# Performance work log

Hardware: AMD Instinct MI355X
Metric: run time of the kernel (lower is better)

The kernel has to match this reference:

```python
import jax, jax.numpy as jnp
import numpy as np


def setup_inputs() -> dict:
    key = jax.random.key(0)
    ks = jax.random.split(key, 5)
    Bsz, T, d = 8, 2048, 1024
    x = jax.random.normal(ks[0], (Bsz, T, d), dtype=jnp.float32)
    W_in = jax.random.normal(ks[1], (d, d), dtype=jnp.float32) * (1.0 / np.sqrt(d))
    b_in = jnp.zeros((d,), dtype=jnp.float32)
    log_A = -jnp.ones((d,), dtype=jnp.float32)  # keras Constant(-1.0) init
    B_vec = jax.random.normal(ks[2], (d,), dtype=jnp.float32) * 0.05  # keras random_normal stddev
    C = jax.random.normal(ks[3], (d, d), dtype=jnp.float32) * 0.05
    D = jnp.zeros((d,), dtype=jnp.float32)
    return {"x": x, "W_in": W_in, "b_in": b_in, "log_A": log_A, "B_vec": B_vec, "C": C, "D": D}


def reference(x, W_in, b_in, log_A, B_vec, C, D):
    # u = in_proj(x)
    u = jnp.einsum('btd,de->bte', x, W_in) + b_in            # [B,T,d]
    A = -jnp.exp(log_A)                                       # [d]
    # linear recurrence h_t = h_{t-1} * A + u_t * B, h_0 = 0
    # expressed as an associative scan over pairs (a_t, b_t):
    #   (a1,b1) o (a2,b2) = (a1*a2, b1*a2 + b2)
    b = u * B_vec                                             # [B,T,d]
    a = jnp.broadcast_to(A, b.shape)                          # [B,T,d]

    def combine(e1, e2):
        a1, b1 = e1
        a2, b2 = e2
        return (a1 * a2, b1 * a2 + b2)

    _, h_seq = jax.lax.associative_scan(combine, (a, b), axis=1)  # h_t, [B,T,d]
    y = jnp.einsum('bts,sd->btd', h_seq, C)
    return y + x * D
```

## Files before the change

### kernel.cpp

```cpp
#include <hip/hip_runtime.h>
#include <hip/hip_bf16.h>

typedef unsigned short ushort_t;
typedef __bf16 bf16x8 __attribute__((ext_vector_type(8)));
typedef float f32x4 __attribute__((ext_vector_type(4)));

#define BM 128
#define BN 128
#define BK 64

__device__ __forceinline__ float bf2f(ushort_t u) {
    union { unsigned int i; float f; } x; x.i = ((unsigned int)u) << 16; return x.f;
}
__device__ __forceinline__ ushort_t f2bf(float f) {
    __hip_bfloat16 h = __float2bfloat16(f);
    return *(ushort_t*)&h;
}
__device__ __forceinline__ void async16(const void* g, void* l) {
    __builtin_amdgcn_global_load_lds((const __attribute__((address_space(1))) void*)g,
                                     (__attribute__((address_space(3))) void*)l, 16, 0, 0);
}

__global__ void prep_fused(const float* __restrict__ x, const float* __restrict__ W_in,
                           const float* __restrict__ C, const float* __restrict__ Bv,
                           __hip_bfloat16* __restrict__ xb, __hip_bfloat16* __restrict__ Wpt,
                           __hip_bfloat16* __restrict__ Ct) {
    int bid = blockIdx.x;
    if (bid < 16384) {
        size_t idx = ((size_t)bid * 256 + threadIdx.x) * 4;
        float4 v = *(const float4*)(x + idx);
        ushort4 ov;
        ov.x = f2bf(v.x); ov.y = f2bf(v.y); ov.z = f2bf(v.z); ov.w = f2bf(v.w);
        *(ushort4*)((ushort_t*)xb + idx) = ov;
        return;
    }
    __shared__ float tile[32][33];
    const float* in;
    __hip_bfloat16* out;
    bool do_scale;
    int lid;
    if (bid < 17408) { lid = bid - 16384; in = W_in; out = Wpt; do_scale = true; }
    else             { lid = bid - 17408; in = C;    out = Ct;  do_scale = false; }
    int bx = (lid & 31) * 32;
    int by = (lid >> 5) * 32;
    int tx = threadIdx.x & 31, ty = threadIdx.x >> 5;
    #pragma unroll
    for (int i = 0; i < 32; i += 8)
        tile[ty + i][tx] = in[(size_t)(by + ty + i) * 1024 + bx + tx];
    __syncthreads();
    if (threadIdx.x < 128) {
        int n_local = threadIdx.x & 31;
        int quad    = threadIdx.x >> 5;
        int n = bx + n_local;
        float s = do_scale ? Bv[n] : 1.0f;
        int lr     = n & 15;
        int n_tile = n >> 4;
        int k_tile = by >> 5;
        ushort_t buf[8];
        #pragma unroll
        for (int j = 0; j < 8; ++j)
            buf[j] = f2bf(tile[quad * 8 + j][n_local] * s);
        size_t off = (((size_t)n_tile * 32 + k_tile) * 64 + quad * 16 + lr) * 8;
        ushort_t* dst = (ushort_t*)out + off;
        *(ushort4*)dst       = *(ushort4*)&buf[0];
        *(ushort4*)(dst + 4) = *(ushort4*)&buf[4];
    }
}

__global__ __launch_bounds__(256) void gemm1_scan(
    const __hip_bfloat16* __restrict__ Ab, const __hip_bfloat16* __restrict__ Bpk,
    const float* __restrict__ b_in, const float* __restrict__ Bv,
    const float* __restrict__ logA,
    __hip_bfloat16* __restrict__ hout, int M, int N, int K) {
    const int tid  = threadIdx.x;
    const int wave = tid >> 6;
    const int lane = tid & 63;
    const int quad = lane >> 4;
    const int lr   = lane & 15;
    const int wm   = wave >> 1;
    const int wn   = wave & 1;

    const int lin   = blockIdx.y * gridDim.x + blockIdx.x;
    const int xcd   = lin & 7;
    const int local = lin >> 3;
    const int m_blk = xcd * 16 + (local >> 3);
    const int n_blk = local & 7;
    const int m0 = m_blk * BM;
    const int n0 = n_blk * BN;

    __shared__ __align__(16) ushort_t sBuf[160 * 136];

    const ushort_t* A  = (const ushort_t*)Ab;
    const ushort_t* Bp = (const ushort_t*)Bpk;
    const int ktiles = K >> 5;
    const int ntile0 = n0 >> 4;

    f32x4 acc[5][4];
    #pragma unroll
    for (int i = 0; i < 5; ++i)
        #pragma unroll
        for (int j = 0; j < 4; ++j)
            #pragma unroll
            for (int r = 0; r < 4; ++r) acc[i][j][r] = 0.0f;

    const int row8 = lane >> 3;
    const int schunk = (lane & 7) ^ row8;
    const int ldcol = schunk * 8;
    for (int k0 = 0; k0 < K; k0 += BK) {
        __syncthreads();
        #pragma unroll
        for (int j = 0; j < 5; ++j) {
            int c = j * 4 + wave;
            int row = c * 8 + row8;
            int grow = m0 - 32 + row;
            if (grow < 0) grow = 0;
            const ushort_t* gA = A + (size_t)grow * K + k0 + ldcol;
            async16(gA, &sBuf[c * 512]);
        }
        __syncthreads();
        #pragma unroll
        for (int kk = 0; kk < BK; kk += 32) {
            const int kt = (k0 + kk) >> 5;
            bf16x8 bfr[4];
            #pragma unroll
            for (int j = 0; j < 4; ++j)
                bfr[j] = *(const bf16x8*)&Bp[((((size_t)(ntile0 + wn * 4 + j)) * ktiles + kt) * 64 + lane) * 8];
            const int ck = (kk >> 3) + quad;
            const int pc = (ck ^ (lr & 7)) * 8;
            bf16x8 af[5];
            #pragma unroll
            for (int i = 0; i < 5; ++i)
                af[i] = *(const bf16x8*)&sBuf[(wm * 80 + i * 16 + lr) * BK + pc];
            #pragma unroll
            for (int i = 0; i < 5; ++i)
                #pragma unroll
                for (int j = 0; j < 4; ++j)
                    acc[i][j] = __builtin_amdgcn_mfma_f32_16x16x32_bf16(af[i], bfr[j], acc[i][j], 0, 0, 0);
        }
    }

    __syncthreads();
    #pragma unroll
    for (int i = 0; i < 5; ++i)
        #pragma unroll
        for (int j = 0; j < 4; ++j) {
            int colL = wn * 64 + j * 16 + lr;
            float bs = b_in[n0 + colL] * Bv[n0 + colL];
            #pragma unroll
            for (int r = 0; r < 4; ++r) {
                int slot = wm * 80 + i * 16 + quad * 4 + r;
                sBuf[slot * 136 + colL] = f2bf(acc[i][j][r] + bs);
            }
        }
    __syncthreads();
    if (tid < 128) {
        float a = -__expf(logA[n0 + tid]);
        float h = 0.f;
        int s = ((m0 & 2047) == 0) ? 32 : 0;
        for (; s < 32; ++s)
            h = fmaf(a, h, bf2f(sBuf[s * 136 + tid]));
        #pragma unroll 4
        for (int t = 32; t < 160; ++t) {
            h = fmaf(a, h, bf2f(sBuf[t * 136 + tid]));
            sBuf[t * 136 + tid] = f2bf(h);
        }
    }
    __syncthreads();
    #pragma unroll
    for (int i = 0; i < 4; ++i) {
        int r32 = tid >> 3;
        int cch = (tid & 7) * 16;
        int slot = 32 + i * 32 + r32;
        bf16x8 v0 = *(const bf16x8*)&sBuf[slot * 136 + cch];
        bf16x8 v1 = *(const bf16x8*)&sBuf[slot * 136 + cch + 8];
        ushort_t* dst = (ushort_t*)hout + (size_t)(m0 + i * 32 + r32) * N + n0 + cch;
        *(bf16x8*)dst       = v0;
        *(bf16x8*)(dst + 8) = v1;
    }
}

__global__ __launch_bounds__(256) void gemm2(
    const __hip_bfloat16* __restrict__ Ab, const __hip_bfloat16* __restrict__ Bpk,
    const __hip_bfloat16* __restrict__ xres_bf, const float* __restrict__ Dvec,
    float* __restrict__ out_f, int M, int N, int K) {
    const int tid  = threadIdx.x;
    const int wave = tid >> 6;
    const int lane = tid & 63;
    const int quad = lane >> 4;
    const int lr   = lane & 15;
    const int wm   = wave >> 1;
    const int wn   = wave & 1;

    const int lin   = blockIdx.y * gridDim.x + blockIdx.x;
    const int xcd   = lin & 7;
    const int local = lin >> 3;
    const int m_blk = xcd * 16 + (local >> 3);
    const int n_blk = local & 7;
    const int m0 = m_blk * BM;
    const int n0 = n_blk * BN;

    __shared__ __align__(16) ushort_t sA[BM * BK];

    const ushort_t* A  = (const ushort_t*)Ab;
    const ushort_t* Bp = (const ushort_t*)Bpk;
    const int ktiles = K >> 5;
    const int ntile0 = n0 >> 4;

    f32x4 acc[4][4];
    #pragma unroll
    for (int i = 0; i < 4; ++i)
        #pragma unroll
        for (int j = 0; j < 4; ++j)
            #pragma unroll
            for (int r = 0; r < 4; ++r) acc[i][j][r] = 0.0f;

    const int row8 = lane >> 3;
    const int schunk = (lane & 7) ^ row8;
    const int ldcol = schunk * 8;
    for (int k0 = 0; k0 < K; k0 += BK) {
        __syncthreads();
        #pragma unroll
        for (int j = 0; j < 4; ++j) {
            int c = j * 4 + wave;
            int row = c * 8 + row8;
            const ushort_t* gA = A + (size_t)(m0 + row) * K + k0 + ldcol;
            async16(gA, &sA[c * 512]);
        }
        __syncthreads();
        #pragma unroll
        for (int kk = 0; kk < BK; kk += 32) {
            const int kt = (k0 + kk) >> 5;
            bf16x8 bfr[4];
            #pragma unroll
            for (int j = 0; j < 4; ++j)
                bfr[j] = *(const bf16x8*)&Bp[((((size_t)(ntile0 + wn * 4 + j)) * ktiles + kt) * 64 + lane) * 8];
            const int ck = (kk >> 3) + quad;
            const int pc = (ck ^ (lr & 7)) * 8;
            bf16x8 af[4];
            #pragma unroll
            for (int i = 0; i < 4; ++i)
                af[i] = *(const bf16x8*)&sA[(wm * 64 + i * 16 + lr) * BK + pc];
            #pragma unroll
            for (int i = 0; i < 4; ++i)
                #pragma unroll
                for (int j = 0; j < 4; ++j)
                    acc[i][j] = __builtin_amdgcn_mfma_f32_16x16x32_bf16(af[i], bfr[j], acc[i][j], 0, 0, 0);
        }
    }

    #pragma unroll
    for (int i = 0; i < 4; ++i) {
        int row = m0 + wm * 64 + i * 16 + quad * 4;
        #pragma unroll
        for (int j = 0; j < 4; ++j) {
            int col = n0 + wn * 64 + j * 16 + lr;
            float dv = Dvec[col];
            #pragma unroll
            for (int r = 0; r < 4; ++r) {
                float xv = bf2f(((const ushort_t*)xres_bf)[(size_t)(row + r) * N + col]);
                out_f[(size_t)(row + r) * N + col] = acc[i][j][r] + xv * dv;
            }
        }
    }
}

extern "C" void kernel_launch(void* const* d_in, const int* in_sizes, int n_in,
                              void* d_out, int out_size, void* d_ws, size_t ws_size,
                              hipStream_t stream) {
    const float* x    = (const float*)d_in[0];
    const float* W_in = (const float*)d_in[1];
    const float* b_in = (const float*)d_in[2];
    const float* logA = (const float*)d_in[3];
    const float* Bv   = (const float*)d_in[4];
    const float* C    = (const float*)d_in[5];
    const float* Dv   = (const float*)d_in[6];
    float* out = (float*)d_out;

    const int Bsz = 8, T = 2048, d = 1024;
    const int M = Bsz * T;

    char* w = (char*)d_ws;
    __hip_bfloat16* xb   = (__hip_bfloat16*)w;
    __hip_bfloat16* Wpt  = xb + (size_t)M * d;
    __hip_bfloat16* Ct   = Wpt + (size_t)d * d;
    __hip_bfloat16* hbuf = Ct + (size_t)d * d;

    prep_fused<<<16384 + 2048, 256, 0, stream>>>(x, W_in, C, Bv, xb, Wpt, Ct);

    gemm1_scan<<<dim3(d / BN, M / BM), 256, 0, stream>>>(
        xb, Wpt, b_in, Bv, logA, hbuf, M, d, d);
    gemm2<<<dim3(d / BN, M / BM), 256, 0, stream>>>(
        hbuf, Ct, xb, Dv, out, M, d, d);
}
```

Before: 241.3 us.

## Pre-pack activations into MFMA fragment layout and drop LDS staging in GEMMs

The prep kernel now writes x as bf16 in a pre-tiled MFMA fragment layout, and gemm1_scan likewise writes h in that layout. Both GEMMs can then load A and B fragments straight from global memory with contiguous 16-byte per-lane loads, with no LDS staging and no __syncthreads in the K loop. gemm2 reads the fp32 x residual directly instead of the bf16 copy. This removes LDS traffic and barriers, but makes A-tile reuse across waves rely on the L2 cache, and the residual read becomes twice as large.

```diff
diff --git a/kernel.cpp b/kernel.cpp
--- a/kernel.cpp
+++ b/kernel.cpp
@@ -5,10 +5,6 @@
 typedef __bf16 bf16x8 __attribute__((ext_vector_type(8)));
 typedef float f32x4 __attribute__((ext_vector_type(4)));
 
-#define BM 128
-#define BN 128
-#define BK 64
-
 __device__ __forceinline__ float bf2f(ushort_t u) {
     union { unsigned int i; float f; } x; x.i = ((unsigned int)u) << 16; return x.f;
 }
@@ -16,22 +12,35 @@
     __hip_bfloat16 h = __float2bfloat16(f);
     return *(ushort_t*)&h;
 }
-__device__ __forceinline__ void async16(const void* g, void* l) {
-    __builtin_amdgcn_global_load_lds((const __attribute__((address_space(1))) void*)g,
-                                     (__attribute__((address_space(3))) void*)l, 16, 0, 0);
-}
+
 
 __global__ void prep_fused(const float* __restrict__ x, const float* __restrict__ W_in,
                            const float* __restrict__ C, const float* __restrict__ Bv,
-                           __hip_bfloat16* __restrict__ xb, __hip_bfloat16* __restrict__ Wpt,
+                           __hip_bfloat16* __restrict__ xpk, __hip_bfloat16* __restrict__ Wpt,
                            __hip_bfloat16* __restrict__ Ct) {
     int bid = blockIdx.x;
-    if (bid < 16384) {
-        size_t idx = ((size_t)bid * 256 + threadIdx.x) * 4;
-        float4 v = *(const float4*)(x + idx);
-        ushort4 ov;
-        ov.x = f2bf(v.x); ov.y = f2bf(v.y); ov.z = f2bf(v.z); ov.w = f2bf(v.w);
-        *(ushort4*)((ushort_t*)xb + idx) = ov;
+    if (bid < 1024) {
+        __shared__ ushort_t sm[16 * 1032];
+        int tid = threadIdx.x;
+        #pragma unroll
+        for (int r = 0; r < 16; ++r) {
+            float4 v = *(const float4*)(x + ((size_t)(bid * 16 + r)) * 1024 + tid * 4);
+            ushort4 ov;
+            ov.x = f2bf(v.x); ov.y = f2bf(v.y); ov.z = f2bf(v.z); ov.w = f2bf(v.w);
+            *(ushort4*)&sm[r * 1032 + tid * 4] = ov;
+        }
+        __syncthreads();
+        int lane = tid & 63;
+        int quad = lane >> 4;
+        int lr   = lane & 15;
+        #pragma unroll
+        for (int p = 0; p < 8; ++p) {
+            int kt = p * 4 + (tid >> 6);
+            const ushort_t* src = &sm[lr * 1032 + kt * 32 + quad * 8];
+            ushort_t* dst = (ushort_t*)xpk + (((size_t)bid * 32 + kt) * 64 + lane) * 8;
+            *(ushort4*)dst       = *(const ushort4*)src;
+            *(ushort4*)(dst + 4) = *(const ushort4*)(src + 4);
+        }
         return;
     }
     __shared__ float tile[32][33];
@@ -39,8 +48,8 @@
     __hip_bfloat16* out;
     bool do_scale;
     int lid;
-    if (bid < 17408) { lid = bid - 16384; in = W_in; out = Wpt; do_scale = true; }
-    else             { lid = bid - 17408; in = C;    out = Ct;  do_scale = false; }
+    if (bid < 2048) { lid = bid - 1024; in = W_in; out = Wpt; do_scale = true; }
+    else            { lid = bid - 2048; in = C;    out = Ct;  do_scale = false; }
     int bx = (lid & 31) * 32;
     int by = (lid >> 5) * 32;
     int tx = threadIdx.x & 31, ty = threadIdx.x >> 5;
@@ -68,10 +77,10 @@
 }
 
 __global__ __launch_bounds__(256) void gemm1_scan(
-    const __hip_bfloat16* __restrict__ Ab, const __hip_bfloat16* __restrict__ Bpk,
+    const __hip_bfloat16* __restrict__ Apk, const __hip_bfloat16* __restrict__ Bpk,
     const float* __restrict__ b_in, const float* __restrict__ Bv,
     const float* __restrict__ logA,
-    __hip_bfloat16* __restrict__ hout, int M, int N, int K) {
+    __hip_bfloat16* __restrict__ hpk, int N) {
     const int tid  = threadIdx.x;
     const int wave = tid >> 6;
     const int lane = tid & 63;
@@ -85,15 +94,27 @@
     const int local = lin >> 3;
     const int m_blk = xcd * 16 + (local >> 3);
     const int n_blk = local & 7;
-    const int m0 = m_blk * BM;
-    const int n0 = n_blk * BN;
+    const int m0 = m_blk * 128;
+    const int n0 = n_blk * 128;
 
     __shared__ __align__(16) ushort_t sBuf[160 * 136];
 
-    const ushort_t* A  = (const ushort_t*)Ab;
+    const ushort_t* Ap = (const ushort_t*)Apk;
     const ushort_t* Bp = (const ushort_t*)Bpk;
-    const int ktiles = K >> 5;
-    const int ntile0 = n0 >> 4;
+
+    const ushort_t* pA[5];
+    const ushort_t* pB[4];
+    #pragma unroll
+    for (int i = 0; i < 5; ++i) {
+        int mt = (m0 >> 4) - 2 + wm * 5 + i;
+        if (mt < 0) mt = 0;
+        pA[i] = Ap + (size_t)mt * 32 * 512 + lane * 8;
+    }
+    #pragma unroll
+    for (int j = 0; j < 4; ++j) {
+        int nt = (n0 >> 4) + wn * 4 + j;
+        pB[j] = Bp + (size_t)nt * 32 * 512 + lane * 8;
+    }
 
     f32x4 acc[5][4];
     #pragma unroll
@@ -103,40 +124,18 @@
             #pragma unroll
             for (int r = 0; r < 4; ++r) acc[i][j][r] = 0.0f;
 
-    const int row8 = lane >> 3;
-    const int schunk = (lane & 7) ^ row8;
-    const int ldcol = schunk * 8;
-    for (int k0 = 0; k0 < K; k0 += BK) {
-        __syncthreads();
-        #pragma unroll
-        for (int j = 0; j < 5; ++j) {
-            int c = j * 4 + wave;
-            int row = c * 8 + row8;
-            int grow = m0 - 32 + row;
-            if (grow < 0) grow = 0;
-            const ushort_t* gA = A + (size_t)grow * K + k0 + ldcol;
-            async16(gA, &sBuf[c * 512]);
-        }
-        __syncthreads();
-        #pragma unroll
-        for (int kk = 0; kk < BK; kk += 32) {
-            const int kt = (k0 + kk) >> 5;
-            bf16x8 bfr[4];
+    #pragma unroll 2
+    for (int kt = 0; kt < 32; ++kt) {
+        bf16x8 af[5], bfr[4];
+        #pragma unroll
+        for (int i = 0; i < 5; ++i) af[i]  = *(const bf16x8*)(pA[i] + (size_t)kt * 512);
+        #pragma unroll
+        for (int j = 0; j < 4; ++j) bfr[j] = *(const bf16x8*)(pB[j] + (size_t)kt * 512);
+        #pragma unroll
+        for (int i = 0; i < 5; ++i)
             #pragma unroll
             for (int j = 0; j < 4; ++j)
-                bfr[j] = *(const bf16x8*)&Bp[((((size_t)(ntile0 + wn * 4 + j)) * ktiles + kt) * 64 + lane) * 8];
-            const int ck = (kk >> 3) + quad;
-            const int pc = (ck ^ (lr & 7)) * 8;
-            bf16x8 af[5];
-            #pragma unroll
-            for (int i = 0; i < 5; ++i)
-                af[i] = *(const bf16x8*)&sBuf[(wm * 80 + i * 16 + lr) * BK + pc];
-            #pragma unroll
-            for (int i = 0; i < 5; ++i)
-                #pragma unroll
-                for (int j = 0; j < 4; ++j)
-                    acc[i][j] = __builtin_amdgcn_mfma_f32_16x16x32_bf16(af[i], bfr[j], acc[i][j], 0, 0, 0);
-        }
+                acc[i][j] = __builtin_amdgcn_mfma_f32_16x16x32_bf16(af[i], bfr[j], acc[i][j], 0, 0, 0);
     }
 
     __syncthreads();
@@ -167,22 +166,23 @@
     }
     __syncthreads();
     #pragma unroll
-    for (int i = 0; i < 4; ++i) {
-        int r32 = tid >> 3;
-        int cch = (tid & 7) * 16;
-        int slot = 32 + i * 32 + r32;
-        bf16x8 v0 = *(const bf16x8*)&sBuf[slot * 136 + cch];
-        bf16x8 v1 = *(const bf16x8*)&sBuf[slot * 136 + cch + 8];
-        ushort_t* dst = (ushort_t*)hout + (size_t)(m0 + i * 32 + r32) * N + n0 + cch;
-        *(bf16x8*)dst       = v0;
-        *(bf16x8*)(dst + 8) = v1;
+    for (int p = 0; p < 8; ++p) {
+        int sb   = p * 4 + wave;
+        int mt_l = sb >> 2;
+        int kt_l = sb & 3;
+        const ushort_t* src = &sBuf[(32 + mt_l * 16 + lr) * 136 + kt_l * 32 + quad * 8];
+        size_t mt  = (size_t)((m0 >> 4) + mt_l);
+        size_t kt2 = (size_t)((n0 >> 5) + kt_l);
+        ushort_t* dst = (ushort_t*)hpk + ((mt * 32 + kt2) * 64 + lane) * 8;
+        *(ushort4*)dst       = *(const ushort4*)src;
+        *(ushort4*)(dst + 4) = *(const ushort4*)(src + 4);
     }
 }
 
 __global__ __launch_bounds__(256) void gemm2(
-    const __hip_bfloat16* __restrict__ Ab, const __hip_bfloat16* __restrict__ Bpk,
-    const __hip_bfloat16* __restrict__ xres_bf, const float* __restrict__ Dvec,
-    float* __restrict__ out_f, int M, int N, int K) {
+    const __hip_bfloat16* __restrict__ Apk, const __hip_bfloat16* __restrict__ Bpk,
+    const float* __restrict__ xres_f, const float* __restrict__ Dvec,
+    float* __restrict__ out_f, int N) {
     const int tid  = threadIdx.x;
     const int wave = tid >> 6;
     const int lane = tid & 63;
@@ -196,15 +196,20 @@
     const int local = lin >> 3;
     const int m_blk = xcd * 16 + (local >> 3);
     const int n_blk = local & 7;
-    const int m0 = m_blk * BM;
-    const int n0 = n_blk * BN;
-
-    __shared__ __align__(16) ushort_t sA[BM * BK];
-
-    const ushort_t* A  = (const ushort_t*)Ab;
+    const int m0 = m_blk * 128;
+    const int n0 = n_blk * 128;
+
+    const ushort_t* Ap = (const ushort_t*)Apk;
     const ushort_t* Bp = (const ushort_t*)Bpk;
-    const int ktiles = K >> 5;
-    const int ntile0 = n0 >> 4;
+
+    const ushort_t* pA[4];
+    const ushort_t* pB[4];
+    #pragma unroll
+    for (int i = 0; i < 4; ++i)
+        pA[i] = Ap + (size_t)((m0 >> 4) + wm * 4 + i) * 32 * 512 + lane * 8;
+    #pragma unroll
+    for (int j = 0; j < 4; ++j)
+        pB[j] = Bp + (size_t)((n0 >> 4) + wn * 4 + j) * 32 * 512 + lane * 8;
 
     f32x4 acc[4][4];
     #pragma unroll
@@ -214,38 +219,18 @@
             #pragma unroll
             for (int r = 0; r < 4; ++r) acc[i][j][r] = 0.0f;
 
-    const int row8 = lane >> 3;
-    const int schunk = (lane & 7) ^ row8;
-    const int ldcol = schunk * 8;
-    for (int k0 = 0; k0 < K; k0 += BK) {
-        __syncthreads();
-        #pragma unroll
-        for (int j = 0; j < 4; ++j) {
-            int c = j * 4 + wave;
-            int row = c * 8 + row8;
-            const ushort_t* gA = A + (size_t)(m0 + row) * K + k0 + ldcol;
-            async16(gA, &sA[c * 512]);
-        }
-        __syncthreads();
-        #pragma unroll
-        for (int kk = 0; kk < BK; kk += 32) {
-            const int kt = (k0 + kk) >> 5;
-            bf16x8 bfr[4];
+    #pragma unroll 2
+    for (int kt = 0; kt < 32; ++kt) {
+        bf16x8 af[4], bfr[4];
+        #pragma unroll
+        for (int i = 0; i < 4; ++i) af[i]  = *(const bf16x8*)(pA[i] + (size_t)kt * 512);
+        #pragma unroll
+        for (int j = 0; j < 4; ++j) bfr[j] = *(const bf16x8*)(pB[j] + (size_t)kt * 512);
+        #pragma unroll
+        for (int i = 0; i < 4; ++i)
             #pragma unroll
             for (int j = 0; j < 4; ++j)
-                bfr[j] = *(const bf16x8*)&Bp[((((size_t)(ntile0 + wn * 4 + j)) * ktiles + kt) * 64 + lane) * 8];
-            const int ck = (kk >> 3) + quad;
-            const int pc = (ck ^ (lr & 7)) * 8;
-            bf16x8 af[4];
-            #pragma unroll
-            for (int i = 0; i < 4; ++i)
-                af[i] = *(const bf16x8*)&sA[(wm * 64 + i * 16 + lr) * BK + pc];
-            #pragma unroll
-            for (int i = 0; i < 4; ++i)
-                #pragma unroll
-                for (int j = 0; j < 4; ++j)
-                    acc[i][j] = __builtin_amdgcn_mfma_f32_16x16x32_bf16(af[i], bfr[j], acc[i][j], 0, 0, 0);
-        }
+                acc[i][j] = __builtin_amdgcn_mfma_f32_16x16x32_bf16(af[i], bfr[j], acc[i][j], 0, 0, 0);
     }
 
     #pragma unroll
@@ -257,7 +242,7 @@
             float dv = Dvec[col];
             #pragma unroll
             for (int r = 0; r < 4; ++r) {
-                float xv = bf2f(((const ushort_t*)xres_bf)[(size_t)(row + r) * N + col]);
+                float xv = xres_f[(size_t)(row + r) * N + col];
                 out_f[(size_t)(row + r) * N + col] = acc[i][j][r] + xv * dv;
             }
         }
@@ -280,15 +265,15 @@
     const int M = Bsz * T;
 
     char* w = (char*)d_ws;
-    __hip_bfloat16* xb   = (__hip_bfloat16*)w;
-    __hip_bfloat16* Wpt  = xb + (size_t)M * d;
-    __hip_bfloat16* Ct   = Wpt + (size_t)d * d;
-    __hip_bfloat16* hbuf = Ct + (size_t)d * d;
-
-    prep_fused<<<16384 + 2048, 256, 0, stream>>>(x, W_in, C, Bv, xb, Wpt, Ct);
-
-    gemm1_scan<<<dim3(d / BN, M / BM), 256, 0, stream>>>(
-        xb, Wpt, b_in, Bv, logA, hbuf, M, d, d);
-    gemm2<<<dim3(d / BN, M / BM), 256, 0, stream>>>(
-        hbuf, Ct, xb, Dv, out, M, d, d);
-}
+    __hip_bfloat16* xpk = (__hip_bfloat16*)w;
+    __hip_bfloat16* Wpt = xpk + (size_t)M * d;
+    __hip_bfloat16* Ct  = Wpt + (size_t)d * d;
+    __hip_bfloat16* hpk = Ct + (size_t)d * d;
+
+    prep_fused<<<3072, 256, 0, stream>>>(x, W_in, C, Bv, xpk, Wpt, Ct);
+
+    gemm1_scan<<<dim3(8, 128), 256, 0, stream>>>(
+        xpk, Wpt, b_in, Bv, logA, hpk, d);
+    gemm2<<<dim3(8, 128), 256, 0, stream>>>(
+        hpk, Ct, x, Dv, out, d);
+}
```

New measurement: 244.5 us. Within noise of the previous version (+1.3%).
